# Kernel optimization log

Measured on AMD Instinct MI355X. Metric: run time of the kernel, lower is better.

Reference implementation:

```python
import jax, jax.numpy as jnp
import numpy as np

C = 4096  # d_model (RWKV-7B scale)


def setup_inputs() -> dict:
    key = jax.random.key(0)
    ks = jax.random.split(key, 14)
    vec = lambda k: jax.random.normal(k, (C,), dtype=jnp.float32)
    mat = lambda k: jax.random.normal(k, (C, C), dtype=jnp.float32) * 0.02
    return {
        "x": vec(ks[0]),
        "state": vec(ks[1]),
        "state_a": vec(ks[2]),
        # state_b is a running sum of exponentials in RWKV -> strictly positive
        "state_b": jax.random.uniform(ks[3], (C,), dtype=jnp.float32) + 0.5,
        "state_p": vec(ks[4]),
        "time_mix_k": jax.random.uniform(ks[5], (C,), dtype=jnp.float32),
        "time_mix_v": jax.random.uniform(ks[6], (C,), dtype=jnp.float32),
        "time_mix_r": jax.random.uniform(ks[7], (C,), dtype=jnp.float32),
        "time_first": vec(ks[8]) * 0.5,
        # time_decay is negative in RWKV (exp decay of the state)
        "time_decay": -jnp.abs(vec(ks[9])) - 0.1,
        "kw": mat(ks[10]),
        "vw": mat(ks[11]),
        "rw": mat(ks[12]),
        "ow": mat(ks[13]),
    }


def reference(x, state, state_a, state_b, state_p,
              time_mix_k, time_mix_v, time_mix_r,
              time_first, time_decay, kw, vw, rw, ow):
    # token-shift interpolation with previous token (state)
    xk = x * time_mix_k + state * (1.0 - time_mix_k)
    xv = x * time_mix_v + state * (1.0 - time_mix_v)
    xr = x * time_mix_r + state * (1.0 - time_mix_r)
    new_state = x

    r = jax.nn.sigmoid(rw @ xr)   # [C]
    kk = kw @ xk                  # [C]
    vv = vw @ xv                  # [C]

    aa, bb, pp = state_a, state_b, state_p

    # output accumulators with max-trick stabilization
    ww = time_first + kk
    p = jnp.maximum(pp, ww)
    e1 = jnp.exp(pp - p)
    e2 = jnp.exp(ww - p)
    a = e1 * aa + e2 * vv
    b = e1 * bb + e2

    # state update (decayed accumulators)
    ww = pp + time_decay
    p = jnp.maximum(ww, kk)
    e1 = jnp.exp(ww - p)
    e2 = jnp.exp(kk - p)
    new_state_a = e1 * aa + e2 * vv
    new_state_b = e1 * bb + e2
    new_state_p = p

    wkv = a / b
    out = ow @ (r * wkv)
    return (out, new_state, new_state_a, new_state_b, new_state_p)
```

## Files before the change

### kernel.cpp

```cpp
#include <hip/hip_runtime.h>
#include <math.h>

#define C 4096

__global__ __launch_bounds__(256) void matvec3_kernel(
    const float* __restrict__ kw, const float* __restrict__ vw, const float* __restrict__ rw,
    const float* __restrict__ x, const float* __restrict__ state,
    const float* __restrict__ tmk, const float* __restrict__ tmv, const float* __restrict__ tmr,
    float* __restrict__ kk, float* __restrict__ vvo, float* __restrict__ rr) {
    __shared__ float4 xs[C / 4];

    const int t = threadIdx.x;
    const int m = blockIdx.x >> 10;

    const float* W;
    const float* tm;
    float* out;
    if (m == 0)      { W = kw; tm = tmk; out = kk;  }
    else if (m == 1) { W = vw; tm = tmv; out = vvo; }
    else             { W = rw; tm = tmr; out = rr;  }

    const float4* x4 = (const float4*)x;
    const float4* s4 = (const float4*)state;
    const float4* t4 = (const float4*)tm;
#pragma unroll
    for (int j = 0; j < 4; ++j) {
        int i = j * 256 + t;
        float4 xi = x4[i], si = s4[i], ti = t4[i];
        float4 r;
        r.x = xi.x * ti.x + si.x * (1.0f - ti.x);
        r.y = xi.y * ti.y + si.y * (1.0f - ti.y);
        r.z = xi.z * ti.z + si.z * (1.0f - ti.z);
        r.w = xi.w * ti.w + si.w * (1.0f - ti.w);
        xs[i] = r;
    }
    __syncthreads();

    const int wave = t >> 6;
    const int lane = t & 63;
    const int row  = (blockIdx.x & 1023) * 4 + wave;
    const float4* Wrow = (const float4*)(W + (size_t)row * C);

    float4 wreg[16];
#pragma unroll
    for (int it = 0; it < 16; ++it) wreg[it] = Wrow[it * 64 + lane];

    float s0 = 0.f, s1 = 0.f, s2 = 0.f, s3 = 0.f;
#pragma unroll
    for (int it = 0; it < 16; ++it) {
        float4 xx = xs[it * 64 + lane];
        float4 w  = wreg[it];
        s0 += w.x * xx.x;
        s1 += w.y * xx.y;
        s2 += w.z * xx.z;
        s3 += w.w * xx.w;
    }
    float sum = (s0 + s1) + (s2 + s3);
#pragma unroll
    for (int off = 32; off > 0; off >>= 1) sum += __shfl_down(sum, off, 64);
    if (lane == 0) out[row] = sum;
}

__global__ void wkv_kernel(const float* __restrict__ kk, const float* __restrict__ vv,
                           const float* __restrict__ rr,
                           const float* __restrict__ aa, const float* __restrict__ bb,
                           const float* __restrict__ pp,
                           const float* __restrict__ time_first,
                           const float* __restrict__ time_decay,
                           const float* __restrict__ x,
                           float* __restrict__ rwkv,
                           float* __restrict__ new_state,
                           float* __restrict__ out_sa, float* __restrict__ out_sb,
                           float* __restrict__ out_sp) {
    int i = blockIdx.x * blockDim.x + threadIdx.x;
    if (i < C) {
        float k = kk[i], v = vv[i];
        float a_ = aa[i], b_ = bb[i], p_ = pp[i];

        float ww = time_first[i] + k;
        float p  = fmaxf(p_, ww);
        float e1 = expf(p_ - p);
        float e2 = expf(ww - p);
        float a  = e1 * a_ + e2 * v;
        float b  = e1 * b_ + e2;

        float ww2 = p_ + time_decay[i];
        float p2  = fmaxf(ww2, k);
        float e1b = expf(ww2 - p2);
        float e2b = expf(k - p2);
        out_sa[i] = e1b * a_ + e2b * v;
        out_sb[i] = e1b * b_ + e2b;
        out_sp[i] = p2;

        new_state[i] = x[i];

        float r = 1.0f / (1.0f + expf(-rr[i]));
        rwkv[i] = r * (a / b);
    }
}

__global__ __launch_bounds__(256) void matvec_kernel(const float* __restrict__ W,
                                                     const float* __restrict__ xin,
                                                     float* __restrict__ out) {
    __shared__ float4 xs[C / 4];
    const int t = threadIdx.x;

    const float4* x4 = (const float4*)xin;
#pragma unroll
    for (int j = 0; j < 4; ++j) {
        int i = j * 256 + t;
        xs[i] = x4[i];
    }
    __syncthreads();

    const int wave = t >> 6;
    const int lane = t & 63;
    const int row  = blockIdx.x * 4 + wave;
    const float4* Wrow = (const float4*)(W + (size_t)row * C);

    float4 wreg[16];
#pragma unroll
    for (int it = 0; it < 16; ++it) wreg[it] = Wrow[it * 64 + lane];

    float s0 = 0.f, s1 = 0.f, s2 = 0.f, s3 = 0.f;
#pragma unroll
    for (int it = 0; it < 16; ++it) {
        float4 xx = xs[it * 64 + lane];
        float4 w  = wreg[it];
        s0 += w.x * xx.x;
        s1 += w.y * xx.y;
        s2 += w.z * xx.z;
        s3 += w.w * xx.w;
    }
    float sum = (s0 + s1) + (s2 + s3);
#pragma unroll
    for (int off = 32; off > 0; off >>= 1) sum += __shfl_down(sum, off, 64);
    if (lane == 0) out[row] = sum;
}

extern "C" void kernel_launch(void* const* d_in, const int* in_sizes, int n_in,
                              void* d_out, int out_size, void* d_ws, size_t ws_size,
                              hipStream_t stream) {
    const float* x          = (const float*)d_in[0];
    const float* state      = (const float*)d_in[1];
    const float* state_a    = (const float*)d_in[2];
    const float* state_b    = (const float*)d_in[3];
    const float* state_p    = (const float*)d_in[4];
    const float* tmk        = (const float*)d_in[5];
    const float* tmv        = (const float*)d_in[6];
    const float* tmr        = (const float*)d_in[7];
    const float* time_first = (const float*)d_in[8];
    const float* time_decay = (const float*)d_in[9];
    const float* kw         = (const float*)d_in[10];
    const float* vw         = (const float*)d_in[11];
    const float* rw         = (const float*)d_in[12];
    const float* ow         = (const float*)d_in[13];

    float* out       = (float*)d_out;
    float* new_state = out + C;
    float* new_sa    = out + 2 * C;
    float* new_sb    = out + 3 * C;
    float* new_sp    = out + 4 * C;

    float* ws   = (float*)d_ws;
    float* kk   = ws;
    float* vv   = ws + C;
    float* rr   = ws + 2 * C;
    float* rwkv = ws + 3 * C;

    matvec3_kernel<<<3 * C / 4, 256, 0, stream>>>(kw, vw, rw, x, state, tmk, tmv, tmr,
                                                  kk, vv, rr);

    wkv_kernel<<<C / 256, 256, 0, stream>>>(kk, vv, rr, state_a, state_b, state_p,
                                            time_first, time_decay, x,
                                            rwkv, new_state, new_sa, new_sb, new_sp);

    matvec_kernel<<<C / 4, 256, 0, stream>>>(ow, rwkv, out);
}
```

Measured before the change: 258.0 us.

## Fuse k/v/r matvecs with WKV elementwise and process multiple rows per wave

```diff
diff --git a/kernel.cpp b/kernel.cpp
--- a/kernel.cpp
+++ b/kernel.cpp
@@ -3,107 +3,153 @@
 
 #define C 4096
 
-__global__ __launch_bounds__(256) void matvec3_kernel(
+__global__ __launch_bounds__(256) void fused_kvr_wkv_kernel(
     const float* __restrict__ kw, const float* __restrict__ vw, const float* __restrict__ rw,
     const float* __restrict__ x, const float* __restrict__ state,
     const float* __restrict__ tmk, const float* __restrict__ tmv, const float* __restrict__ tmr,
-    float* __restrict__ kk, float* __restrict__ vvo, float* __restrict__ rr) {
-    __shared__ float4 xs[C / 4];
+    const float* __restrict__ aa, const float* __restrict__ bb, const float* __restrict__ pp,
+    const float* __restrict__ time_first, const float* __restrict__ time_decay,
+    float* __restrict__ rwkv, float* __restrict__ new_state,
+    float* __restrict__ out_sa, float* __restrict__ out_sb, float* __restrict__ out_sp)
+{
+    __shared__ float4 xsk[C / 4];
+    __shared__ float4 xsv[C / 4];
+    __shared__ float4 xsr[C / 4];
+    __shared__ float  part[3][8][2];
 
     const int t = threadIdx.x;
-    const int m = blockIdx.x >> 10;
-
-    const float* W;
-    const float* tm;
-    float* out;
-    if (m == 0)      { W = kw; tm = tmk; out = kk;  }
-    else if (m == 1) { W = vw; tm = tmv; out = vvo; }
-    else             { W = rw; tm = tmr; out = rr;  }
-
-    const float4* x4 = (const float4*)x;
-    const float4* s4 = (const float4*)state;
-    const float4* t4 = (const float4*)tm;
+    const int R = blockIdx.x * 8;
+
+    const float4* x4  = (const float4*)x;
+    const float4* s4  = (const float4*)state;
+    const float4* tk4 = (const float4*)tmk;
+    const float4* tv4 = (const float4*)tmv;
+    const float4* tr4 = (const float4*)tmr;
 #pragma unroll
     for (int j = 0; j < 4; ++j) {
         int i = j * 256 + t;
-        float4 xi = x4[i], si = s4[i], ti = t4[i];
-        float4 r;
-        r.x = xi.x * ti.x + si.x * (1.0f - ti.x);
-        r.y = xi.y * ti.y + si.y * (1.0f - ti.y);
-        r.z = xi.z * ti.z + si.z * (1.0f - ti.z);
-        r.w = xi.w * ti.w + si.w * (1.0f - ti.w);
-        xs[i] = r;
+        float4 xi = x4[i], si = s4[i];
+        float4 mk = tk4[i], mv = tv4[i], mr = tr4[i];
+        float4 rk, rv, rr;
+        rk.x = si.x + mk.x * (xi.x - si.x);
+        rk.y = si.y + mk.y * (xi.y - si.y);
+        rk.z = si.z + mk.z * (xi.z - si.z);
+        rk.w = si.w + mk.w * (xi.w - si.w);
+        rv.x = si.x + mv.x * (xi.x - si.x);
+        rv.y = si.y + mv.y * (xi.y - si.y);
+        rv.z = si.z + mv.z * (xi.z - si.z);
+        rv.w = si.w + mv.w * (xi.w - si.w);
+        rr.x = si.x + mr.x * (xi.x - si.x);
+        rr.y = si.y + mr.y * (xi.y - si.y);
+        rr.z = si.z + mr.z * (xi.z - si.z);
+        rr.w = si.w + mr.w * (xi.w - si.w);
+        xsk[i] = rk; xsv[i] = rv; xsr[i] = rr;
     }
     __syncthreads();
 
     const int wave = t >> 6;
     const int lane = t & 63;
-    const int row  = (blockIdx.x & 1023) * 4 + wave;
-    const float4* Wrow = (const float4*)(W + (size_t)row * C);
-
-    float4 wreg[16];
-#pragma unroll
-    for (int it = 0; it < 16; ++it) wreg[it] = Wrow[it * 64 + lane];
-
-    float s0 = 0.f, s1 = 0.f, s2 = 0.f, s3 = 0.f;
-#pragma unroll
-    for (int it = 0; it < 16; ++it) {
-        float4 xx = xs[it * 64 + lane];
-        float4 w  = wreg[it];
-        s0 += w.x * xx.x;
-        s1 += w.y * xx.y;
-        s2 += w.z * xx.z;
-        s3 += w.w * xx.w;
-    }
-    float sum = (s0 + s1) + (s2 + s3);
-#pragma unroll
-    for (int off = 32; off > 0; off >>= 1) sum += __shfl_down(sum, off, 64);
-    if (lane == 0) out[row] = sum;
-}
-
-__global__ void wkv_kernel(const float* __restrict__ kk, const float* __restrict__ vv,
-                           const float* __restrict__ rr,
-                           const float* __restrict__ aa, const float* __restrict__ bb,
-                           const float* __restrict__ pp,
-                           const float* __restrict__ time_first,
-                           const float* __restrict__ time_decay,
-                           const float* __restrict__ x,
-                           float* __restrict__ rwkv,
-                           float* __restrict__ new_state,
-                           float* __restrict__ out_sa, float* __restrict__ out_sb,
-                           float* __restrict__ out_sp) {
-    int i = blockIdx.x * blockDim.x + threadIdx.x;
-    if (i < C) {
-        float k = kk[i], v = vv[i];
+    const int h    = wave & 1;
+    const int rg   = wave >> 1;
+    const int r0   = R + rg * 4;
+
+    const float4* pk0 = (const float4*)(kw + (size_t)(r0 + 0) * C);
+    const float4* pk1 = (const float4*)(kw + (size_t)(r0 + 1) * C);
+    const float4* pk2 = (const float4*)(kw + (size_t)(r0 + 2) * C);
+    const float4* pk3 = (const float4*)(kw + (size_t)(r0 + 3) * C);
+    const float4* pv0 = (const float4*)(vw + (size_t)(r0 + 0) * C);
+    const float4* pv1 = (const float4*)(vw + (size_t)(r0 + 1) * C);
+    const float4* pv2 = (const float4*)(vw + (size_t)(r0 + 2) * C);
+    const float4* pv3 = (const float4*)(vw + (size_t)(r0 + 3) * C);
+    const float4* pr0 = (const float4*)(rw + (size_t)(r0 + 0) * C);
+    const float4* pr1 = (const float4*)(rw + (size_t)(r0 + 1) * C);
+    const float4* pr2 = (const float4*)(rw + (size_t)(r0 + 2) * C);
+    const float4* pr3 = (const float4*)(rw + (size_t)(r0 + 3) * C);
+
+    float ak0 = 0.f, ak1 = 0.f, ak2 = 0.f, ak3 = 0.f;
+    float av0 = 0.f, av1 = 0.f, av2 = 0.f, av3 = 0.f;
+    float ar0 = 0.f, ar1 = 0.f, ar2 = 0.f, ar3 = 0.f;
+
+    const int cb0 = h * 512 + lane;
+#pragma unroll 2
+    for (int it = 0; it < 8; ++it) {
+        const int cb = cb0 + it * 64;
+        float4 wk0 = pk0[cb]; float4 wk1 = pk1[cb]; float4 wk2 = pk2[cb]; float4 wk3 = pk3[cb];
+        float4 wv0 = pv0[cb]; float4 wv1 = pv1[cb]; float4 wv2 = pv2[cb]; float4 wv3 = pv3[cb];
+        float4 wr0 = pr0[cb]; float4 wr1 = pr1[cb]; float4 wr2 = pr2[cb]; float4 wr3 = pr3[cb];
+        float4 xk_ = xsk[cb]; float4 xv_ = xsv[cb]; float4 xr_ = xsr[cb];
+        ak0 += wk0.x * xk_.x + wk0.y * xk_.y + wk0.z * xk_.z + wk0.w * xk_.w;
+        ak1 += wk1.x * xk_.x + wk1.y * xk_.y + wk1.z * xk_.z + wk1.w * xk_.w;
+        ak2 += wk2.x * xk_.x + wk2.y * xk_.y + wk2.z * xk_.z + wk2.w * xk_.w;
+        ak3 += wk3.x * xk_.x + wk3.y * xk_.y + wk3.z * xk_.z + wk3.w * xk_.w;
+        av0 += wv0.x * xv_.x + wv0.y * xv_.y + wv0.z * xv_.z + wv0.w * xv_.w;
+        av1 += wv1.x * xv_.x + wv1.y * xv_.y + wv1.z * xv_.z + wv1.w * xv_.w;
+        av2 += wv2.x * xv_.x + wv2.y * xv_.y + wv2.z * xv_.z + wv2.w * xv_.w;
+        av3 += wv3.x * xv_.x + wv3.y * xv_.y + wv3.z * xv_.z + wv3.w * xv_.w;
+        ar0 += wr0.x * xr_.x + wr0.y * xr_.y + wr0.z * xr_.z + wr0.w * xr_.w;
+        ar1 += wr1.x * xr_.x + wr1.y * xr_.y + wr1.z * xr_.z + wr1.w * xr_.w;
+        ar2 += wr2.x * xr_.x + wr2.y * xr_.y + wr2.z * xr_.z + wr2.w * xr_.w;
+        ar3 += wr3.x * xr_.x + wr3.y * xr_.y + wr3.z * xr_.z + wr3.w * xr_.w;
+    }
+
+#define WREDUCE(s) do { \
+        s += __shfl_down(s, 32, 64); s += __shfl_down(s, 16, 64); \
+        s += __shfl_down(s,  8, 64); s += __shfl_down(s,  4, 64); \
+        s += __shfl_down(s,  2, 64); s += __shfl_down(s,  1, 64); } while (0)
+    WREDUCE(ak0); WREDUCE(ak1); WREDUCE(ak2); WREDUCE(ak3);
+    WREDUCE(av0); WREDUCE(av1); WREDUCE(av2); WREDUCE(av3);
+    WREDUCE(ar0); WREDUCE(ar1); WREDUCE(ar2); WREDUCE(ar3);
+#undef WREDUCE
+
+    if (lane == 0) {
+        part[0][rg * 4 + 0][h] = ak0; part[0][rg * 4 + 1][h] = ak1;
+        part[0][rg * 4 + 2][h] = ak2; part[0][rg * 4 + 3][h] = ak3;
+        part[1][rg * 4 + 0][h] = av0; part[1][rg * 4 + 1][h] = av1;
+        part[1][rg * 4 + 2][h] = av2; part[1][rg * 4 + 3][h] = av3;
+        part[2][rg * 4 + 0][h] = ar0; part[2][rg * 4 + 1][h] = ar1;
+        part[2][rg * 4 + 2][h] = ar2; part[2][rg * 4 + 3][h] = ar3;
+    }
+    __syncthreads();
+
+    if (t < 8) {
+        const int i = R + t;
+        float kk = part[0][t][0] + part[0][t][1];
+        float vv = part[1][t][0] + part[1][t][1];
+        float rr = part[2][t][0] + part[2][t][1];
+
         float a_ = aa[i], b_ = bb[i], p_ = pp[i];
 
-        float ww = time_first[i] + k;
+        float ww = time_first[i] + kk;
         float p  = fmaxf(p_, ww);
         float e1 = expf(p_ - p);
         float e2 = expf(ww - p);
-        float a  = e1 * a_ + e2 * v;
+        float a  = e1 * a_ + e2 * vv;
         float b  = e1 * b_ + e2;
 
         float ww2 = p_ + time_decay[i];
-        float p2  = fmaxf(ww2, k);
+        float p2  = fmaxf(ww2, kk);
         float e1b = expf(ww2 - p2);
-        float e2b = expf(k - p2);
-        out_sa[i] = e1b * a_ + e2b * v;
+        float e2b = expf(kk - p2);
+        out_sa[i] = e1b * a_ + e2b * vv;
         out_sb[i] = e1b * b_ + e2b;
         out_sp[i] = p2;
 
         new_state[i] = x[i];
 
-        float r = 1.0f / (1.0f + expf(-rr[i]));
+        float r = 1.0f / (1.0f + expf(-rr));
         rwkv[i] = r * (a / b);
     }
 }
 
-__global__ __launch_bounds__(256) void matvec_kernel(const float* __restrict__ W,
-                                                     const float* __restrict__ xin,
-                                                     float* __restrict__ out) {
+__global__ __launch_bounds__(256) void ow_kernel(const float* __restrict__ W,
+                                                 const float* __restrict__ xin,
+                                                 float* __restrict__ out)
+{
     __shared__ float4 xs[C / 4];
+    __shared__ float  part[8][2];
+
     const int t = threadIdx.x;
+    const int R = blockIdx.x * 8;
 
     const float4* x4 = (const float4*)xin;
 #pragma unroll
@@ -115,27 +161,44 @@
 
     const int wave = t >> 6;
     const int lane = t & 63;
-    const int row  = blockIdx.x * 4 + wave;
-    const float4* Wrow = (const float4*)(W + (size_t)row * C);
-
-    float4 wreg[16];
-#pragma unroll
-    for (int it = 0; it < 16; ++it) wreg[it] = Wrow[it * 64 + lane];
-
-    float s0 = 0.f, s1 = 0.f, s2 = 0.f, s3 = 0.f;
-#pragma unroll
-    for (int it = 0; it < 16; ++it) {
-        float4 xx = xs[it * 64 + lane];
-        float4 w  = wreg[it];
-        s0 += w.x * xx.x;
-        s1 += w.y * xx.y;
-        s2 += w.z * xx.z;
-        s3 += w.w * xx.w;
-    }
-    float sum = (s0 + s1) + (s2 + s3);
-#pragma unroll
-    for (int off = 32; off > 0; off >>= 1) sum += __shfl_down(sum, off, 64);
-    if (lane == 0) out[row] = sum;
+    const int h    = wave & 1;
+    const int rg   = wave >> 1;
+    const int r0   = R + rg * 4;
+
+    const float4* p0 = (const float4*)(W + (size_t)(r0 + 0) * C);
+    const float4* p1 = (const float4*)(W + (size_t)(r0 + 1) * C);
+    const float4* p2 = (const float4*)(W + (size_t)(r0 + 2) * C);
+    const float4* p3 = (const float4*)(W + (size_t)(r0 + 3) * C);
+
+    float a0 = 0.f, a1 = 0.f, a2 = 0.f, a3 = 0.f;
+    const int cb0 = h * 512 + lane;
+#pragma unroll 2
+    for (int it = 0; it < 8; ++it) {
+        const int cb = cb0 + it * 64;
+        float4 w0 = p0[cb]; float4 w1 = p1[cb]; float4 w2 = p2[cb]; float4 w3 = p3[cb];
+        float4 xx = xs[cb];
+        a0 += w0.x * xx.x + w0.y * xx.y + w0.z * xx.z + w0.w * xx.w;
+        a1 += w1.x * xx.x + w1.y * xx.y + w1.z * xx.z + w1.w * xx.w;
+        a2 += w2.x * xx.x + w2.y * xx.y + w2.z * xx.z + w2.w * xx.w;
+        a3 += w3.x * xx.x + w3.y * xx.y + w3.z * xx.z + w3.w * xx.w;
+    }
+
+#define WREDUCE(s) do { \
+        s += __shfl_down(s, 32, 64); s += __shfl_down(s, 16, 64); \
+        s += __shfl_down(s,  8, 64); s += __shfl_down(s,  4, 64); \
+        s += __shfl_down(s,  2, 64); s += __shfl_down(s,  1, 64); } while (0)
+    WREDUCE(a0); WREDUCE(a1); WREDUCE(a2); WREDUCE(a3);
+#undef WREDUCE
+
+    if (lane == 0) {
+        part[rg * 4 + 0][h] = a0;
+        part[rg * 4 + 1][h] = a1;
+        part[rg * 4 + 2][h] = a2;
+        part[rg * 4 + 3][h] = a3;
+    }
+    __syncthreads();
+
+    if (t < 8) out[R + t] = part[t][0] + part[t][1];
 }
 
 extern "C" void kernel_launch(void* const* d_in, const int* in_sizes, int n_in,
@@ -162,18 +225,12 @@
     float* new_sb    = out + 3 * C;
     float* new_sp    = out + 4 * C;
 
-    float* ws   = (float*)d_ws;
-    float* kk   = ws;
-    float* vv   = ws + C;
-    float* rr   = ws + 2 * C;
-    float* rwkv = ws + 3 * C;
-
-    matvec3_kernel<<<3 * C / 4, 256, 0, stream>>>(kw, vw, rw, x, state, tmk, tmv, tmr,
-                                                  kk, vv, rr);
-
-    wkv_kernel<<<C / 256, 256, 0, stream>>>(kk, vv, rr, state_a, state_b, state_p,
-                                            time_first, time_decay, x,
-                                            rwkv, new_state, new_sa, new_sb, new_sp);
-
-    matvec_kernel<<<C / 4, 256, 0, stream>>>(ow, rwkv, out);
+    float* rwkv = (float*)d_ws;
+
+    fused_kvr_wkv_kernel<<<C / 8, 256, 0, stream>>>(
+        kw, vw, rw, x, state, tmk, tmv, tmr,
+        state_a, state_b, state_p, time_first, time_decay,
+        rwkv, new_state, new_sa, new_sb, new_sp);
+
+    ow_kernel<<<C / 8, 256, 0, stream>>>(ow, rwkv, out);
 }
```

Measured after the change: 265.4 us. 2.9% more time.

## Fuse k/v/r GEMVs with WKV update and software-pipeline weight loads

Applied to the files above, without the earlier changes.

```diff
diff --git a/kernel.cpp b/kernel.cpp
--- a/kernel.cpp
+++ b/kernel.cpp
@@ -2,108 +2,121 @@
 #include <math.h>
 
 #define C 4096
+#define NF4 (C / 4)
 
-__global__ __launch_bounds__(256) void matvec3_kernel(
+__global__ __launch_bounds__(256) void gemv_kvr_wkv_kernel(
     const float* __restrict__ kw, const float* __restrict__ vw, const float* __restrict__ rw,
     const float* __restrict__ x, const float* __restrict__ state,
     const float* __restrict__ tmk, const float* __restrict__ tmv, const float* __restrict__ tmr,
-    float* __restrict__ kk, float* __restrict__ vvo, float* __restrict__ rr) {
-    __shared__ float4 xs[C / 4];
+    const float* __restrict__ aa, const float* __restrict__ bb, const float* __restrict__ pp,
+    const float* __restrict__ time_first, const float* __restrict__ time_decay,
+    float* __restrict__ rwkv, float* __restrict__ new_state,
+    float* __restrict__ out_sa, float* __restrict__ out_sb, float* __restrict__ out_sp)
+{
+    __shared__ float4 xs[NF4];
 
-    const int t = threadIdx.x;
-    const int m = blockIdx.x >> 10;
-
-    const float* W;
-    const float* tm;
-    float* out;
-    if (m == 0)      { W = kw; tm = tmk; out = kk;  }
-    else if (m == 1) { W = vw; tm = tmv; out = vvo; }
-    else             { W = rw; tm = tmr; out = rr;  }
+    const int t    = threadIdx.x;
+    const int wave = t >> 6;
+    const int lane = t & 63;
+    const int row  = blockIdx.x * 4 + wave;
 
     const float4* x4 = (const float4*)x;
     const float4* s4 = (const float4*)state;
-    const float4* t4 = (const float4*)tm;
+
+    float kk_r = 0.f, vv_r = 0.f, rr_r = 0.f;
+
 #pragma unroll
-    for (int j = 0; j < 4; ++j) {
-        int i = j * 256 + t;
-        float4 xi = x4[i], si = s4[i], ti = t4[i];
-        float4 r;
-        r.x = xi.x * ti.x + si.x * (1.0f - ti.x);
-        r.y = xi.y * ti.y + si.y * (1.0f - ti.y);
-        r.z = xi.z * ti.z + si.z * (1.0f - ti.z);
-        r.w = xi.w * ti.w + si.w * (1.0f - ti.w);
-        xs[i] = r;
+    for (int m = 0; m < 3; ++m) {
+        const float* W  = (m == 0) ? kw  : (m == 1) ? vw  : rw;
+        const float* Tm = (m == 0) ? tmk : (m == 1) ? tmv : tmr;
+
+        __syncthreads();
+        const float4* t4 = (const float4*)Tm;
+#pragma unroll
+        for (int j = 0; j < 4; ++j) {
+            int i = j * 256 + t;
+            float4 xi = x4[i], si = s4[i], ti = t4[i];
+            float4 r;
+            r.x = si.x + ti.x * (xi.x - si.x);
+            r.y = si.y + ti.y * (xi.y - si.y);
+            r.z = si.z + ti.z * (xi.z - si.z);
+            r.w = si.w + ti.w * (xi.w - si.w);
+            xs[i] = r;
+        }
+        __syncthreads();
+
+        const float4* Wp = (const float4*)(W + (size_t)row * C);
+
+        float4 w0 = Wp[lane +   0];
+        float4 w1 = Wp[lane +  64];
+        float4 w2 = Wp[lane + 128];
+        float4 w3 = Wp[lane + 192];
+        float a0 = 0.f, a1 = 0.f, a2 = 0.f, a3 = 0.f;
+#pragma unroll
+        for (int g = 0; g < 4; ++g) {
+            const int b = g * 256 + lane;
+            float4 n0 = make_float4(0.f, 0.f, 0.f, 0.f);
+            float4 n1 = n0, n2 = n0, n3 = n0;
+            if (g < 3) {
+                n0 = Wp[b + 256];
+                n1 = Wp[b + 320];
+                n2 = Wp[b + 384];
+                n3 = Wp[b + 448];
+            }
+            float4 x0 = xs[b], x1 = xs[b + 64], x2 = xs[b + 128], x3 = xs[b + 192];
+            a0 += w0.x * x0.x + w0.y * x0.y + w0.z * x0.z + w0.w * x0.w;
+            a1 += w1.x * x1.x + w1.y * x1.y + w1.z * x1.z + w1.w * x1.w;
+            a2 += w2.x * x2.x + w2.y * x2.y + w2.z * x2.z + w2.w * x2.w;
+            a3 += w3.x * x3.x + w3.y * x3.y + w3.z * x3.z + w3.w * x3.w;
+            w0 = n0; w1 = n1; w2 = n2; w3 = n3;
+        }
+        float s = (a0 + a1) + (a2 + a3);
+        s += __shfl_down(s, 32, 64);
+        s += __shfl_down(s, 16, 64);
+        s += __shfl_down(s,  8, 64);
+        s += __shfl_down(s,  4, 64);
+        s += __shfl_down(s,  2, 64);
+        s += __shfl_down(s,  1, 64);
+        if (m == 0) kk_r = s; else if (m == 1) vv_r = s; else rr_r = s;
     }
-    __syncthreads();
 
-    const int wave = t >> 6;
-    const int lane = t & 63;
-    const int row  = (blockIdx.x & 1023) * 4 + wave;
-    const float4* Wrow = (const float4*)(W + (size_t)row * C);
-
-    float4 wreg[16];
-#pragma unroll
-    for (int it = 0; it < 16; ++it) wreg[it] = Wrow[it * 64 + lane];
-
-    float s0 = 0.f, s1 = 0.f, s2 = 0.f, s3 = 0.f;
-#pragma unroll
-    for (int it = 0; it < 16; ++it) {
-        float4 xx = xs[it * 64 + lane];
-        float4 w  = wreg[it];
-        s0 += w.x * xx.x;
-        s1 += w.y * xx.y;
-        s2 += w.z * xx.z;
-        s3 += w.w * xx.w;
-    }
-    float sum = (s0 + s1) + (s2 + s3);
-#pragma unroll
-    for (int off = 32; off > 0; off >>= 1) sum += __shfl_down(sum, off, 64);
-    if (lane == 0) out[row] = sum;
-}
-
-__global__ void wkv_kernel(const float* __restrict__ kk, const float* __restrict__ vv,
-                           const float* __restrict__ rr,
-                           const float* __restrict__ aa, const float* __restrict__ bb,
-                           const float* __restrict__ pp,
-                           const float* __restrict__ time_first,
-                           const float* __restrict__ time_decay,
-                           const float* __restrict__ x,
-                           float* __restrict__ rwkv,
-                           float* __restrict__ new_state,
-                           float* __restrict__ out_sa, float* __restrict__ out_sb,
-                           float* __restrict__ out_sp) {
-    int i = blockIdx.x * blockDim.x + threadIdx.x;
-    if (i < C) {
-        float k = kk[i], v = vv[i];
+    if (lane == 0) {
+        const int i = row;
+        float kk = kk_r, vv = vv_r, rr = rr_r;
         float a_ = aa[i], b_ = bb[i], p_ = pp[i];
 
-        float ww = time_first[i] + k;
+        float ww = time_first[i] + kk;
         float p  = fmaxf(p_, ww);
         float e1 = expf(p_ - p);
         float e2 = expf(ww - p);
-        float a  = e1 * a_ + e2 * v;
+        float a  = e1 * a_ + e2 * vv;
         float b  = e1 * b_ + e2;
 
         float ww2 = p_ + time_decay[i];
-        float p2  = fmaxf(ww2, k);
+        float p2  = fmaxf(ww2, kk);
         float e1b = expf(ww2 - p2);
-        float e2b = expf(k - p2);
-        out_sa[i] = e1b * a_ + e2b * v;
+        float e2b = expf(kk - p2);
+        out_sa[i] = e1b * a_ + e2b * vv;
         out_sb[i] = e1b * b_ + e2b;
         out_sp[i] = p2;
 
         new_state[i] = x[i];
 
-        float r = 1.0f / (1.0f + expf(-rr[i]));
+        float r = 1.0f / (1.0f + expf(-rr));
         rwkv[i] = r * (a / b);
     }
 }
 
-__global__ __launch_bounds__(256) void matvec_kernel(const float* __restrict__ W,
-                                                     const float* __restrict__ xin,
-                                                     float* __restrict__ out) {
-    __shared__ float4 xs[C / 4];
-    const int t = threadIdx.x;
+__global__ __launch_bounds__(256) void gemv_ow_kernel(const float* __restrict__ W,
+                                                      const float* __restrict__ xin,
+                                                      float* __restrict__ out)
+{
+    __shared__ float4 xs[NF4];
+
+    const int t    = threadIdx.x;
+    const int wave = t >> 6;
+    const int lane = t & 63;
+    const int row  = blockIdx.x * 4 + wave;
 
     const float4* x4 = (const float4*)xin;
 #pragma unroll
@@ -113,29 +126,39 @@
     }
     __syncthreads();
 
-    const int wave = t >> 6;
-    const int lane = t & 63;
-    const int row  = blockIdx.x * 4 + wave;
-    const float4* Wrow = (const float4*)(W + (size_t)row * C);
+    const float4* Wp = (const float4*)(W + (size_t)row * C);
 
-    float4 wreg[16];
+    float4 w0 = Wp[lane +   0];
+    float4 w1 = Wp[lane +  64];
+    float4 w2 = Wp[lane + 128];
+    float4 w3 = Wp[lane + 192];
+    float a0 = 0.f, a1 = 0.f, a2 = 0.f, a3 = 0.f;
 #pragma unroll
-    for (int it = 0; it < 16; ++it) wreg[it] = Wrow[it * 64 + lane];
-
-    float s0 = 0.f, s1 = 0.f, s2 = 0.f, s3 = 0.f;
-#pragma unroll
-    for (int it = 0; it < 16; ++it) {
-        float4 xx = xs[it * 64 + lane];
-        float4 w  = wreg[it];
-        s0 += w.x * xx.x;
-        s1 += w.y * xx.y;
-        s2 += w.z * xx.z;
-        s3 += w.w * xx.w;
+    for (int g = 0; g < 4; ++g) {
+        const int b = g * 256 + lane;
+        float4 n0 = make_float4(0.f, 0.f, 0.f, 0.f);
+        float4 n1 = n0, n2 = n0, n3 = n0;
+        if (g < 3) {
+            n0 = Wp[b + 256];
+            n1 = Wp[b + 320];
+            n2 = Wp[b + 384];
+            n3 = Wp[b + 448];
+        }
+        float4 x0 = xs[b], x1 = xs[b + 64], x2 = xs[b + 128], x3 = xs[b + 192];
+        a0 += w0.x * x0.x + w0.y * x0.y + w0.z * x0.z + w0.w * x0.w;
+        a1 += w1.x * x1.x + w1.y * x1.y + w1.z * x1.z + w1.w * x1.w;
+        a2 += w2.x * x2.x + w2.y * x2.y + w2.z * x2.z + w2.w * x2.w;
+        a3 += w3.x * x3.x + w3.y * x3.y + w3.z * x3.z + w3.w * x3.w;
+        w0 = n0; w1 = n1; w2 = n2; w3 = n3;
     }
-    float sum = (s0 + s1) + (s2 + s3);
-#pragma unroll
-    for (int off = 32; off > 0; off >>= 1) sum += __shfl_down(sum, off, 64);
-    if (lane == 0) out[row] = sum;
+    float s = (a0 + a1) + (a2 + a3);
+    s += __shfl_down(s, 32, 64);
+    s += __shfl_down(s, 16, 64);
+    s += __shfl_down(s,  8, 64);
+    s += __shfl_down(s,  4, 64);
+    s += __shfl_down(s,  2, 64);
+    s += __shfl_down(s,  1, 64);
+    if (lane == 0) out[row] = s;
 }
 
 extern "C" void kernel_launch(void* const* d_in, const int* in_sizes, int n_in,
@@ -162,18 +185,12 @@
     float* new_sb    = out + 3 * C;
     float* new_sp    = out + 4 * C;
 
-    float* ws   = (float*)d_ws;
-    float* kk   = ws;
-    float* vv   = ws + C;
-    float* rr   = ws + 2 * C;
-    float* rwkv = ws + 3 * C;
+    float* rwkv = (float*)d_ws;
 
-    matvec3_kernel<<<3 * C / 4, 256, 0, stream>>>(kw, vw, rw, x, state, tmk, tmv, tmr,
-                                                  kk, vv, rr);
+    gemv_kvr_wkv_kernel<<<C / 4, 256, 0, stream>>>(
+        kw, vw, rw, x, state, tmk, tmv, tmr,
+        state_a, state_b, state_p, time_first, time_decay,
+        rwkv, new_state, new_sa, new_sb, new_sp);
 
-    wkv_kernel<<<C / 256, 256, 0, stream>>>(kk, vv, rr, state_a, state_b, state_p,
-                                            time_first, time_decay, x,
-                                            rwkv, new_state, new_sa, new_sb, new_sp);
-
-    matvec_kernel<<<C / 4, 256, 0, stream>>>(ow, rwkv, out);
+    gemv_ow_kernel<<<C / 4, 256, 0, stream>>>(ow, rwkv, out);
 }
```

Measured after the change: 261.7 us. Within noise of the previous version (+1.4%).
